# Kernel optimization log

Measured on AMD Instinct MI355X. Metric: run time of the kernel, lower is better.

Reference implementation:

```python
import jax, jax.numpy as jnp
import numpy as np

N_USERS = 20000
N_ITEMS = 20000
H0, H1, H2 = 256, 512, 256  # hidden = [256, 512, 256]
B = 4096
LN_EPS = 1e-5


def _ln(x, g, b):
    m = jnp.mean(x, axis=-1, keepdims=True)
    v = jnp.mean(jnp.square(x - m), axis=-1, keepdims=True)
    return (x - m) * jax.lax.rsqrt(v + LN_EPS) * g + b


def setup_inputs() -> dict:
    key = jax.random.key(0)
    ks = jax.random.split(key, 12)
    s = 0.02
    inp = {
        "user_idx": jax.random.randint(ks[0], (B,), 0, N_USERS),
        "item_idx": jax.random.randint(ks[1], (B,), 0, N_ITEMS),
        # (n_users+1, n_items+1) binary interaction matrix, stored as bool
        "interactions": jax.random.bernoulli(ks[2], 0.05, (N_USERS + 1, N_ITEMS + 1)),
        # proj_u / proj_i (bias=False), torch Linear layout (out, in)
        "Wu": jax.random.normal(ks[3], (H0, N_ITEMS), jnp.float32) * s,
        "Wi": jax.random.normal(ks[4], (H0, N_USERS), jnp.float32) * s,
        # rep_u: Linear(H0,H1)+LN+ReLU, Linear(H1,H2)+LN+ReLU (dropout=eval identity)
        "W1": jax.random.normal(ks[5], (H1, H0), jnp.float32) * s,
        "b1": jnp.zeros((H1,), jnp.float32),
        "g1": jnp.ones((H1,), jnp.float32),
        "be1": jnp.zeros((H1,), jnp.float32),
        "W2": jax.random.normal(ks[6], (H2, H1), jnp.float32) * s,
        "b2": jnp.zeros((H2,), jnp.float32),
        "g2": jnp.ones((H2,), jnp.float32),
        "be2": jnp.zeros((H2,), jnp.float32),
        # logit layer
        "Wl": jax.random.normal(ks[7], (1, H2), jnp.float32) * s,
        "bl": jnp.zeros((1,), jnp.float32),
    }
    return inp


def reference(user_idx, item_idx, interactions, Wu, Wi, W1, b1, g1, be1,
              W2, b2, g2, be2, Wl, bl):
    b_arange = jnp.arange(user_idx.shape[0])

    # --- user history embedding: gather row, zero target item, project, MLP ---
    u_slice = interactions[user_idx, :-1].astype(jnp.float32)      # (B, n_items)
    u_slice = u_slice.at[b_arange, item_idx].set(0.0)
    u = u_slice @ Wu.T                                             # (B, H0)
    u = jax.nn.relu(_ln(u @ W1.T + b1, g1, be1))                   # (B, H1)
    user_rep = jax.nn.relu(_ln(u @ W2.T + b2, g2, be2))            # (B, H2)

    # --- item history embedding: gather column, zero target user, project ---
    i_slice = interactions.T[item_idx][:, :-1].astype(jnp.float32)  # (B, n_users)
    i_slice = i_slice.at[b_arange, user_idx].set(0.0)
    item_rep = i_slice @ Wi.T                                      # (B, H0); rep_i is an empty Sequential in source

    pred_vector = user_rep * item_rep                              # (B, H2) == (B, H0)
    logit = (pred_vector @ Wl.T + bl).squeeze(-1)                  # (B,)
    return logit
```

## Files before the change

kernel.cpp:

```cpp
#include <hip/hip_runtime.h>

#define N_USERS 20000
#define N_ITEMS 20000
#define NI1     20001
#define HB      4096
#define H0      256
#define H1      512
#define H2      256
#define PKW     632
#define PKB     (PKW*4)
#define NWF     12501251

typedef unsigned short u16;
typedef unsigned char  u8;
typedef unsigned int   u32;
typedef unsigned long long u64;

typedef __attribute__((ext_vector_type(8))) __bf16 bf16x8;
typedef __attribute__((ext_vector_type(4))) float  f32x4;

__device__ __forceinline__ u16 f2bf(float f) {
  u32 u = __float_as_uint(f);
  u32 r = (u + 0x7FFFu + ((u >> 16) & 1u)) >> 16;
  return (u16)r;
}

__global__ __launch_bounds__(256) void k_detect(const u8* __restrict__ inter,
                                                int* __restrict__ flag) {
  __shared__ u32 cnt[4];
  if (threadIdx.x < 4) cnt[threadIdx.x] = 0;
  __syncthreads();
  u32 loc0 = 0, loc1 = 0, loc2 = 0, loc3 = 0;
  for (int i = threadIdx.x; i < 16384; i += 256) {
    u32 w = ((const u32*)inter)[i];
    loc0 += (w & 0x000000FFu) ? 1u : 0u;
    loc1 += (w & 0x0000FF00u) ? 1u : 0u;
    loc2 += (w & 0x00FF0000u) ? 1u : 0u;
    loc3 += (w & 0xFF000000u) ? 1u : 0u;
  }
  atomicAdd(&cnt[0], loc0); atomicAdd(&cnt[1], loc1);
  atomicAdd(&cnt[2], loc2); atomicAdd(&cnt[3], loc3);
  __syncthreads();
  if (threadIdx.x == 0) {
    int lay;
    if (cnt[1] != 0)      lay = 0;
    else if (cnt[0] != 0) lay = 1;
    else                  lay = 2;
    *flag = lay;
  }
}

__global__ __launch_bounds__(256) void k_packF(const u8* __restrict__ inter,
                                               u32* __restrict__ pkF,
                                               const int* __restrict__ flag) {
  int lay = *flag;
  __shared__ u32 nibs[4][8][64];
  const size_t TE = (size_t)NI1 * NI1;
  const int NG = (int)((TE + 8191) / 8192);
  int wave = threadIdx.x >> 6, lane = threadIdx.x & 63;
  const u32* base32 = (const u32*)inter;
  for (int g = blockIdx.x; g < NG; g += gridDim.x) {
    size_t E0 = (size_t)g * 8192 + (size_t)wave * 2048;
    bool full = ((size_t)(g + 1) * 8192) <= TE;
    if (lay != 0) {
      if (full) {
        #pragma unroll
        for (int t = 0; t < 8; ++t) {
          size_t e = E0 + (size_t)t * 256 + lane * 4;
          uint4 v = *(const uint4*)(base32 + e);
          nibs[wave][t][lane] = (v.x ? 1u : 0u) | (v.y ? 2u : 0u) |
                                (v.z ? 4u : 0u) | (v.w ? 8u : 0u);
        }
      } else {
        #pragma unroll
        for (int t = 0; t < 8; ++t) {
          size_t e = E0 + (size_t)t * 256 + lane * 4;
          u32 n = 0;
          #pragma unroll
          for (int c = 0; c < 4; ++c)
            if (e + c < TE && base32[e + c]) n |= 1u << c;
          nibs[wave][t][lane] = n;
        }
      }
    } else {
      #pragma unroll
      for (int t = 0; t < 8; ++t) {
        size_t e = E0 + (size_t)t * 256 + lane * 4;
        u32 n = 0;
        #pragma unroll
        for (int c = 0; c < 4; ++c)
          if (e + c < TE && inter[e + c]) n |= 1u << c;
        nibs[wave][t][lane] = n;
      }
    }
    __syncthreads();
    {
      int t = lane >> 3, j = lane & 7;
      u32 wrd = 0;
      #pragma unroll
      for (int k = 0; k < 8; ++k) wrd |= nibs[wave][t][8 * j + k] << (4 * k);
      size_t wg = (size_t)g * 256 + wave * 64 + lane;
      if (wg < NWF) pkF[wg] = wrd;
    }
    __syncthreads();
  }
}

__global__ __launch_bounds__(256) void k_realign(const u32* __restrict__ pkF,
                                                 u32* __restrict__ pk) {
  int r = blockIdx.x;
  int base = 625 * r + (r >> 5);
  int s = r & 31;
  for (int w = threadIdx.x; w < PKW; w += 256) {
    u32 val = 0;
    if (w < 625) {
      u32 lo = pkF[base + w];
      u32 hi = pkF[base + w + 1];
      val = s ? ((lo >> s) | (hi << (32 - s))) : lo;
    }
    pk[(size_t)r * PKW + w] = val;
  }
}

#define HDSTEP(J, M)                                      \
  _Pragma("unroll")                                       \
  for (int k = 0; k < 32; ++k) if (!(k & J)) {            \
    u32 tt = (a[k] ^ (a[k | J] >> J)) & M;                \
    a[k] ^= tt; a[k | J] ^= tt << J;                      \
  }

__global__ __launch_bounds__(256) void k_bitT(const u32* __restrict__ pk,
                                              u32* __restrict__ pkT) {
  __shared__ u32 in_l[512][17];
  __shared__ u32 out_l[32][16][17];
  int t = threadIdx.x;
  int vt = blockIdx.x % 40, wt = blockIdx.x / 40;
  int v0 = vt * 16, wc0 = wt * 16;
  int lw = t & 15, lr = t >> 4;
  for (int ch = 0; ch < 32; ++ch) {
    int rloc = ch * 16 + lr;
    int R = v0 * 32 + rloc;
    int W = wc0 + lw;
    u32 val = 0;
    if (R < N_USERS && W < PKW) val = pk[(size_t)R * PKW + W];
    in_l[rloc][lw] = val;
  }
  __syncthreads();
  u32 a[32];
  #pragma unroll
  for (int j = 0; j < 32; ++j) a[j] = in_l[lr * 32 + j][lw];
  HDSTEP(16, 0x0000FFFFu)
  HDSTEP(8,  0x00FF00FFu)
  HDSTEP(4,  0x0F0F0F0Fu)
  HDSTEP(2,  0x33333333u)
  HDSTEP(1,  0x55555555u)
  #pragma unroll
  for (int i = 0; i < 32; ++i) out_l[i][lw][lr] = __brev(a[31 - i]);
  __syncthreads();
  for (int ch = 0; ch < 32; ++ch) {
    int rloc = ch * 16 + lr;
    int C = wc0 * 32 + rloc;
    int V = v0 + lw;
    if (C < N_ITEMS && V < PKW)
      pkT[(size_t)C * PKW + V] = out_l[rloc & 31][rloc >> 5][lw];
  }
}

__global__ __launch_bounds__(256) void k_convert2(const float* __restrict__ Wu,
                                                  const float* __restrict__ Wi,
                                                  u16* __restrict__ Wub,
                                                  u16* __restrict__ Wib) {
  const int n4 = H0 * N_ITEMS / 4;
  int stride = gridDim.x * 256;
  for (int i = blockIdx.x * 256 + threadIdx.x; i < 2 * n4; i += stride) {
    const float* in = (i < n4) ? Wu : Wi;
    u16* out = (i < n4) ? Wub : Wib;
    int idx = (i < n4) ? i : i - n4;
    float4 v = ((const float4*)in)[idx];
    u64 p = (u64)f2bf(v.x) | ((u64)f2bf(v.y) << 16) |
            ((u64)f2bf(v.z) << 32) | ((u64)f2bf(v.w) << 48);
    ((u64*)out)[idx] = p;
  }
}

__global__ __launch_bounds__(256) void k_transpose2(const float* __restrict__ W1,
                                                    float* __restrict__ W1T,
                                                    const float* __restrict__ W2,
                                                    float* __restrict__ W2T) {
  __shared__ float tile[32][33];
  int bid = blockIdx.x;
  const float* in; float* out; int R, C, b;
  if (bid < 128) { in = W1; out = W1T; R = H1; C = H0; b = bid; }
  else           { in = W2; out = W2T; R = H2; C = H1; b = bid - 128; }
  int nbx = C >> 5;
  int bx = b % nbx, by = b / nbx;
  int c0 = bx * 32, r0 = by * 32;
  int lx = threadIdx.x & 31, ly = threadIdx.x >> 5;
  #pragma unroll
  for (int j = 0; j < 4; ++j)
    tile[ly + 8*j][lx] = in[(size_t)(r0 + ly + 8*j) * C + c0 + lx];
  __syncthreads();
  #pragma unroll
  for (int j = 0; j < 4; ++j)
    out[(size_t)(c0 + ly + 8*j) * R + r0 + lx] = tile[lx][ly + 8*j];
}

__global__ __launch_bounds__(1024) void k_sort(const int* __restrict__ item_idx,
                                               int* __restrict__ perm) {
  __shared__ u32 cnt[N_ITEMS];
  __shared__ u32 tsum[1024];
  int t = threadIdx.x;
  for (int i = t; i < N_ITEMS; i += 1024) cnt[i] = 0;
  __syncthreads();
  for (int b = t; b < HB; b += 1024) atomicAdd(&cnt[item_idx[b]], 1u);
  __syncthreads();
  u32 s = 0;
  int base = t * 20;
  for (int j = 0; j < 20; ++j) { int i = base + j; if (i < N_ITEMS) s += cnt[i]; }
  tsum[t] = s;
  __syncthreads();
  for (int off = 1; off < 1024; off <<= 1) {
    u32 v = (t >= off) ? tsum[t - off] : 0u;
    __syncthreads();
    tsum[t] += v;
    __syncthreads();
  }
  u32 run = tsum[t] - s;
  for (int j = 0; j < 20; ++j) {
    int i = base + j;
    if (i < N_ITEMS) { u32 c = cnt[i]; cnt[i] = run; run += c; }
  }
  __syncthreads();
  for (int b = t; b < HB; b += 1024) {
    int v = item_idx[b];
    u32 pos = atomicAdd(&cnt[v], 1u);
    perm[pos] = b;
  }
}

__global__ __launch_bounds__(256, 4) void k_gemm(
    const u32* __restrict__ pk, const u32* __restrict__ pkT,
    const int* __restrict__ user_idx, const int* __restrict__ item_idx,
    const int* __restrict__ perm,
    const u16* __restrict__ Wub, const u16* __restrict__ Wib,
    float* __restrict__ u0, float* __restrict__ u0b,
    float* __restrict__ ir, float* __restrict__ irb) {
  __shared__ __attribute__((aligned(16))) u16 Bls[32 * 256];
  __shared__ __attribute__((aligned(16))) uint2 lut8[16];
  __shared__ u32 pbase[128];
  __shared__ int prow[128];

  int bid = blockIdx.x;
  int kh = bid >> 9;
  int mode_item = (bid >> 8) & 1;
  int lid = bid & 255;
  int M0 = (lid >> 3) * 128;
  int N0 = (lid & 7) * 32;
  int tid = threadIdx.x;
  const u16* Wb = mode_item ? Wib : Wub;
  const u8* Pk = (const u8*)(mode_item ? pkT : pk);
  float* Cout = mode_item ? (kh ? irb : ir) : (kh ? u0b : u0);

  if (tid < 16) {
    u32 v = tid;
    lut8[tid].x = ((v & 1u) ? 0x3F80u : 0u) | ((v & 2u) ? 0x3F800000u : 0u);
    lut8[tid].y = ((v & 4u) ? 0x3F80u : 0u) | ((v & 8u) ? 0x3F800000u : 0u);
  }
  if (tid < 128) {
    int s = M0 + tid;
    if (mode_item) { int p = perm[s]; prow[tid] = p; pbase[tid] = (u32)item_idx[p] * PKB; }
    else           { prow[tid] = s;   pbase[tid] = (u32)user_idx[s] * PKB; }
  }
  __syncthreads();

  f32x4 acc[2][2];
  #pragma unroll
  for (int a = 0; a < 2; ++a)
    #pragma unroll
    for (int b = 0; b < 2; ++b)
      #pragma unroll
      for (int j = 0; j < 4; ++j) acc[a][b][j] = 0.f;

  int lane = tid & 63, wave = tid >> 6;
  int WM = wave * 32;
  int lrow = lane & 15;
  int lk8 = lane >> 4;
  int sh = lk8 * 8;

  u32 pb0 = pbase[WM + lrow];
  u32 pb1 = pbase[WM + 16 + lrow];

  int k0_beg = kh ? 10240 : 0;
  int k0_end = kh ? 20224 : 10240;

  for (int k0 = k0_beg; k0 < k0_end; k0 += 256) {
    #pragma unroll
    for (int i = 0; i < 4; ++i) {
      int id = tid + 256 * i;
      int n = id >> 5, c8 = id & 31;
      int k = k0 + c8 * 8;
      uint4 v = make_uint4(0u, 0u, 0u, 0u);
      if (k < N_ITEMS) v = *(const uint4*)&Wb[(size_t)(N0 + n) * N_ITEMS + k];
      int off = n * 256 + ((c8 * 8) ^ ((n & 7) << 3));
      *(uint4*)&Bls[off] = v;
    }
    int bc = k0 >> 3;
    uint4 qa0l = *(const uint4*)(Pk + pb0 + bc);
    uint4 qa0h = *(const uint4*)(Pk + pb0 + bc + 16);
    uint4 qa1l = *(const uint4*)(Pk + pb1 + bc);
    uint4 qa1h = *(const uint4*)(Pk + pb1 + bc + 16);
    u32 qw0[8] = {qa0l.x, qa0l.y, qa0l.z, qa0l.w, qa0h.x, qa0h.y, qa0h.z, qa0h.w};
    u32 qw1[8] = {qa1l.x, qa1l.y, qa1l.z, qa1l.w, qa1h.x, qa1h.y, qa1h.z, qa1h.w};
    __syncthreads();
    #pragma unroll
    for (int kki = 0; kki < 8; ++kki) {
      u32 b0 = (qw0[kki] >> sh) & 0xFFu;
      u32 b1 = (qw1[kki] >> sh) & 0xFFu;
      union { u32 w[4]; bf16x8 v; } a0, a1;
      uint2 l0 = lut8[b0 & 15u], h0 = lut8[b0 >> 4];
      uint2 l1 = lut8[b1 & 15u], h1 = lut8[b1 >> 4];
      a0.w[0] = l0.x; a0.w[1] = l0.y; a0.w[2] = h0.x; a0.w[3] = h0.y;
      a1.w[0] = l1.x; a1.w[1] = l1.y; a1.w[2] = h1.x; a1.w[3] = h1.y;
      bf16x8 bfr[2];
      #pragma unroll
      for (int fn = 0; fn < 2; ++fn) {
        int n = fn * 16 + lrow;
        bfr[fn] = *(const bf16x8*)&Bls[n * 256 + ((kki * 32 + sh) ^ ((n & 7) << 3))];
      }
      acc[0][0] = __builtin_amdgcn_mfma_f32_16x16x32_bf16(a0.v, bfr[0], acc[0][0], 0, 0, 0);
      acc[0][1] = __builtin_amdgcn_mfma_f32_16x16x32_bf16(a0.v, bfr[1], acc[0][1], 0, 0, 0);
      acc[1][0] = __builtin_amdgcn_mfma_f32_16x16x32_bf16(a1.v, bfr[0], acc[1][0], 0, 0, 0);
      acc[1][1] = __builtin_amdgcn_mfma_f32_16x16x32_bf16(a1.v, bfr[1], acc[1][1], 0, 0, 0);
    }
    __syncthreads();
  }

  int crow0 = (lane >> 4) * 4;
  int ccol = lane & 15;
  #pragma unroll
  for (int fm = 0; fm < 2; ++fm)
    #pragma unroll
    for (int fn = 0; fn < 2; ++fn) {
      f32x4 v = acc[fm][fn];
      int col = N0 + fn * 16 + ccol;
      #pragma unroll
      for (int j = 0; j < 4; ++j) {
        int rl = WM + fm * 16 + crow0 + j;
        Cout[(size_t)prow[rl] * H0 + col] = v[j];
      }
    }
}

__global__ __launch_bounds__(256) void k_mlp(
    const u32* __restrict__ pk,
    const int* __restrict__ user_idx, const int* __restrict__ item_idx,
    const float* __restrict__ Wu, const float* __restrict__ Wi,
    const float* __restrict__ u0, const float* __restrict__ u0b,
    const float* __restrict__ ir, const float* __restrict__ irb,
    const float* __restrict__ W1T, const float* __restrict__ b1,
    const float* __restrict__ g1, const float* __restrict__ be1,
    const float* __restrict__ W2T, const float* __restrict__ b2,
    const float* __restrict__ g2, const float* __restrict__ be2,
    const float* __restrict__ Wl, const float* __restrict__ bl,
    float* __restrict__ out) {
  __shared__ __attribute__((aligned(16))) float xl[16][H0];
  __shared__ __attribute__((aligned(16))) float h1l[16][H1];
  __shared__ int flagL[16], uL[16], iL[16];

  int tid = threadIdx.x, lane = tid & 63, wave = tid >> 6;
  int b0 = blockIdx.x * 16;

  if (tid < 16) {
    int b = b0 + tid;
    int uu = user_idx[b], ii = item_idx[b];
    uL[tid] = uu; iL[tid] = ii;
    u8 byte = ((const u8*)pk)[(size_t)uu * PKB + (ii >> 3)];
    flagL[tid] = (byte >> (ii & 7)) & 1;
  }
  __syncthreads();

  for (int idx = tid; idx < 16 * H0; idx += 256) {
    int rr = idx >> 8, h = idx & 255;
    size_t o = (size_t)(b0 + rr) * H0 + h;
    float x = u0[o] + u0b[o];
    if (flagL[rr]) x -= Wu[(size_t)h * N_ITEMS + iL[rr]];
    xl[rr][h] = x;
  }
  __syncthreads();

  float a0[16], a1[16];
  #pragma unroll
  for (int rr = 0; rr < 16; ++rr) { a0[rr] = 0.f; a1[rr] = 0.f; }
  for (int k4 = 0; k4 < H0 / 4; ++k4) {
    int k = k4 * 4;
    float w0a = W1T[(size_t)(k+0)*H1 + tid], w0b = W1T[(size_t)(k+0)*H1 + tid + 256];
    float w1a = W1T[(size_t)(k+1)*H1 + tid], w1b = W1T[(size_t)(k+1)*H1 + tid + 256];
    float w2a = W1T[(size_t)(k+2)*H1 + tid], w2b = W1T[(size_t)(k+2)*H1 + tid + 256];
    float w3a = W1T[(size_t)(k+3)*H1 + tid], w3b = W1T[(size_t)(k+3)*H1 + tid + 256];
    #pragma unroll
    for (int rr = 0; rr < 16; ++rr) {
      float4 x = *(const float4*)&xl[rr][k];
      a0[rr] += x.x * w0a + x.y * w1a + x.z * w2a + x.w * w3a;
      a1[rr] += x.x * w0b + x.y * w1b + x.z * w2b + x.w * w3b;
    }
  }
  #pragma unroll
  for (int rr = 0; rr < 16; ++rr) {
    h1l[rr][tid]       = a0[rr] + b1[tid];
    h1l[rr][tid + 256] = a1[rr] + b1[tid + 256];
  }
  __syncthreads();

  for (int rr = wave; rr < 16; rr += 4) {
    float s = 0.f;
    #pragma unroll
    for (int j = 0; j < 8; ++j) s += h1l[rr][lane + 64 * j];
    #pragma unroll
    for (int off = 32; off; off >>= 1) s += __shfl_xor(s, off);
    float m = s * (1.f / H1);
    float v = 0.f;
    #pragma unroll
    for (int j = 0; j < 8; ++j) { float d = h1l[rr][lane + 64*j] - m; v += d * d; }
    #pragma unroll
    for (int off = 32; off; off >>= 1) v += __shfl_xor(v, off);
    float inv = rsqrtf(v * (1.f / H1) + 1e-5f);
    #pragma unroll
    for (int j = 0; j < 8; ++j) {
      int o = lane + 64 * j;
      float y = (h1l[rr][o] - m) * inv * g1[o] + be1[o];
      h1l[rr][o] = fmaxf(y, 0.f);
    }
  }
  __syncthreads();

  float a2[16];
  #pragma unroll
  for (int rr = 0; rr < 16; ++rr) a2[rr] = 0.f;
  for (int k4 = 0; k4 < H1 / 4; ++k4) {
    int k = k4 * 4;
    float w0 = W2T[(size_t)(k+0)*H2 + tid];
    float w1 = W2T[(size_t)(k+1)*H2 + tid];
    float w2 = W2T[(size_t)(k+2)*H2 + tid];
    float w3 = W2T[(size_t)(k+3)*H2 + tid];
    #pragma unroll
    for (int rr = 0; rr < 16; ++rr) {
      float4 x = *(const float4*)&h1l[rr][k];
      a2[rr] += x.x * w0 + x.y * w1 + x.z * w2 + x.w * w3;
    }
  }
  __syncthreads();
  #pragma unroll
  for (int rr = 0; rr < 16; ++rr) xl[rr][tid] = a2[rr] + b2[tid];
  __syncthreads();

  for (int rr = wave; rr < 16; rr += 4) {
    float s = 0.f;
    #pragma unroll
    for (int j = 0; j < 4; ++j) s += xl[rr][lane + 64 * j];
    #pragma unroll
    for (int off = 32; off; off >>= 1) s += __shfl_xor(s, off);
    float m = s * (1.f / H2);
    float v = 0.f;
    #pragma unroll
    for (int j = 0; j < 4; ++j) { float d = xl[rr][lane + 64*j] - m; v += d * d; }
    #pragma unroll
    for (int off = 32; off; off >>= 1) v += __shfl_xor(v, off);
    float inv = rsqrtf(v * (1.f / H2) + 1e-5f);
    #pragma unroll
    for (int j = 0; j < 4; ++j) {
      int o = lane + 64 * j;
      float y = (xl[rr][o] - m) * inv * g2[o] + be2[o];
      xl[rr][o] = fmaxf(y, 0.f);
    }
  }
  __syncthreads();

  for (int rr = wave; rr < 16; rr += 4) {
    int b = b0 + rr;
    int flg = flagL[rr], uu = uL[rr];
    float s = 0.f;
    #pragma unroll
    for (int j = 0; j < 4; ++j) {
      int h = lane + 64 * j;
      size_t o = (size_t)b * H0 + h;
      float irv = ir[o] + irb[o];
      if (flg) irv -= Wi[(size_t)h * N_USERS + uu];
      s += xl[rr][h] * irv * Wl[h];
    }
    #pragma unroll
    for (int off = 32; off; off >>= 1) s += __shfl_xor(s, off);
    if (lane == 0) out[b] = s + bl[0];
  }
}

extern "C" void kernel_launch(void* const* d_in, const int* in_sizes, int n_in,
                              void* d_out, int out_size, void* d_ws, size_t ws_size,
                              hipStream_t stream) {
  const int*   user_idx = (const int*)d_in[0];
  const int*   item_idx = (const int*)d_in[1];
  const u8*    inter    = (const u8*)d_in[2];
  const float* Wu  = (const float*)d_in[3];
  const float* Wi  = (const float*)d_in[4];
  const float* W1  = (const float*)d_in[5];
  const float* b1  = (const float*)d_in[6];
  const float* g1  = (const float*)d_in[7];
  const float* be1 = (const float*)d_in[8];
  const float* W2  = (const float*)d_in[9];
  const float* b2  = (const float*)d_in[10];
  const float* g2  = (const float*)d_in[11];
  const float* be2 = (const float*)d_in[12];
  const float* Wl  = (const float*)d_in[13];
  const float* bl  = (const float*)d_in[14];
  float* out = (float*)d_out;

  char* ws = (char*)d_ws;
  size_t off = 0;
  auto alloc = [&](size_t bytes) {
    size_t o = off;
    off = (off + bytes + 255) & ~(size_t)255;
    return o;
  };
  int*   flag = (int*)  (ws + alloc(4));
  u32*   pkF  = (u32*)  (ws + alloc((size_t)(NWF + 64) * 4));
  u32*   pk   = (u32*)  (ws + alloc((size_t)N_USERS * PKB));
  u32*   pkT  = (u32*)  (ws + alloc((size_t)N_ITEMS * PKB));
  u16*   Wub  = (u16*)  (ws + alloc((size_t)H0 * N_ITEMS * 2));
  u16*   Wib  = (u16*)  (ws + alloc((size_t)H0 * N_USERS * 2));
  float* W1T  = (float*)(ws + alloc((size_t)H0 * H1 * 4));
  float* W2T  = (float*)(ws + alloc((size_t)H1 * H2 * 4));
  float* u0   = (float*)(ws + alloc((size_t)HB * H0 * 4));
  float* u0b  = (float*)(ws + alloc((size_t)HB * H0 * 4));
  float* ir   = (float*)(ws + alloc((size_t)HB * H0 * 4));
  float* irb  = (float*)(ws + alloc((size_t)HB * H0 * 4));
  int*   perm = (int*)  (ws + alloc((size_t)HB * 4));

  k_detect<<<1, 256, 0, stream>>>(inter, flag);
  k_packF<<<3072, 256, 0, stream>>>(inter, pkF, flag);
  k_realign<<<N_USERS, 256, 0, stream>>>(pkF, pk);
  k_bitT<<<1600, 256, 0, stream>>>(pk, pkT);
  k_convert2<<<1024, 256, 0, stream>>>(Wu, Wi, Wub, Wib);
  k_transpose2<<<256, 256, 0, stream>>>(W1, W1T, W2, W2T);
  k_sort<<<1, 1024, 0, stream>>>(item_idx, perm);
  k_gemm<<<1024, 256, 0, stream>>>(pk, pkT, user_idx, item_idx, perm, Wub, Wib,
                                   u0, u0b, ir, irb);
  k_mlp<<<256, 256, 0, stream>>>(pk, user_idx, item_idx, Wu, Wi, u0, u0b, ir, irb,
                                 W1T, b1, g1, be1, W2T, b2, g2, be2, Wl, bl, out);
}
```

Before: 658.8 us.

## Double-buffer B tile in LDS and prefetch next K-slice into registers

The k_gemm main loop now issues global loads for the next 256-wide K slice of the weight tile and packed interaction bits before running the MFMAs on the current slice. It then writes them into a second LDS buffer, so one barrier per iteration replaces two. This is meant to hide global memory latency behind the MFMA work. In exchange it doubles the B-tile LDS footprint to 32 KB and needs more registers, which may lower occupancy under launch_bounds(256,4).

```diff
diff --git a/kernel.cpp b/kernel.cpp
--- a/kernel.cpp
+++ b/kernel.cpp
@@ -245,7 +245,7 @@
     const u16* __restrict__ Wub, const u16* __restrict__ Wib,
     float* __restrict__ u0, float* __restrict__ u0b,
     float* __restrict__ ir, float* __restrict__ irb) {
-  __shared__ __attribute__((aligned(16))) u16 Bls[32 * 256];
+  __shared__ __attribute__((aligned(16))) u16 Bls[2][32 * 256];
   __shared__ __attribute__((aligned(16))) uint2 lut8[16];
   __shared__ u32 pbase[128];
   __shared__ int prow[128];
@@ -290,28 +290,55 @@
   u32 pb0 = pbase[WM + lrow];
   u32 pb1 = pbase[WM + 16 + lrow];
 
+  int bsn[4], bsk[4], bso[4];
+  #pragma unroll
+  for (int i = 0; i < 4; ++i) {
+    int id = tid + 256 * i;
+    int n = id >> 5, c8 = id & 31;
+    bsn[i] = N0 + n;
+    bsk[i] = c8 * 8;
+    bso[i] = n * 256 + ((c8 * 8) ^ ((n & 7) << 3));
+  }
+
   int k0_beg = kh ? 10240 : 0;
   int k0_end = kh ? 20224 : 10240;
 
+  uint4 breg[4];
+  #pragma unroll
+  for (int i = 0; i < 4; ++i) {
+    int k = k0_beg + bsk[i];
+    breg[i] = make_uint4(0u, 0u, 0u, 0u);
+    if (k < N_ITEMS) breg[i] = *(const uint4*)&Wb[(size_t)bsn[i] * N_ITEMS + k];
+  }
+  #pragma unroll
+  for (int i = 0; i < 4; ++i) *(uint4*)&Bls[0][bso[i]] = breg[i];
+  int bc0 = k0_beg >> 3;
+  uint4 ca0l = *(const uint4*)(Pk + pb0 + bc0);
+  uint4 ca0h = *(const uint4*)(Pk + pb0 + bc0 + 16);
+  uint4 ca1l = *(const uint4*)(Pk + pb1 + bc0);
+  uint4 ca1h = *(const uint4*)(Pk + pb1 + bc0 + 16);
+  __syncthreads();
+
+  int cur = 0;
   for (int k0 = k0_beg; k0 < k0_end; k0 += 256) {
-    #pragma unroll
-    for (int i = 0; i < 4; ++i) {
-      int id = tid + 256 * i;
-      int n = id >> 5, c8 = id & 31;
-      int k = k0 + c8 * 8;
-      uint4 v = make_uint4(0u, 0u, 0u, 0u);
-      if (k < N_ITEMS) v = *(const uint4*)&Wb[(size_t)(N0 + n) * N_ITEMS + k];
-      int off = n * 256 + ((c8 * 8) ^ ((n & 7) << 3));
-      *(uint4*)&Bls[off] = v;
-    }
-    int bc = k0 >> 3;
-    uint4 qa0l = *(const uint4*)(Pk + pb0 + bc);
-    uint4 qa0h = *(const uint4*)(Pk + pb0 + bc + 16);
-    uint4 qa1l = *(const uint4*)(Pk + pb1 + bc);
-    uint4 qa1h = *(const uint4*)(Pk + pb1 + bc + 16);
-    u32 qw0[8] = {qa0l.x, qa0l.y, qa0l.z, qa0l.w, qa0h.x, qa0h.y, qa0h.z, qa0h.w};
-    u32 qw1[8] = {qa1l.x, qa1l.y, qa1l.z, qa1l.w, qa1h.x, qa1h.y, qa1h.z, qa1h.w};
-    __syncthreads();
+    int k1 = k0 + 256;
+    bool more = k1 < k0_end;
+    uint4 na0l, na0h, na1l, na1h;
+    if (more) {
+      #pragma unroll
+      for (int i = 0; i < 4; ++i) {
+        int k = k1 + bsk[i];
+        breg[i] = make_uint4(0u, 0u, 0u, 0u);
+        if (k < N_ITEMS) breg[i] = *(const uint4*)&Wb[(size_t)bsn[i] * N_ITEMS + k];
+      }
+      int nbc = k1 >> 3;
+      na0l = *(const uint4*)(Pk + pb0 + nbc);
+      na0h = *(const uint4*)(Pk + pb0 + nbc + 16);
+      na1l = *(const uint4*)(Pk + pb1 + nbc);
+      na1h = *(const uint4*)(Pk + pb1 + nbc + 16);
+    }
+    u32 qw0[8] = {ca0l.x, ca0l.y, ca0l.z, ca0l.w, ca0h.x, ca0h.y, ca0h.z, ca0h.w};
+    u32 qw1[8] = {ca1l.x, ca1l.y, ca1l.z, ca1l.w, ca1h.x, ca1h.y, ca1h.z, ca1h.w};
     #pragma unroll
     for (int kki = 0; kki < 8; ++kki) {
       u32 b0 = (qw0[kki] >> sh) & 0xFFu;
@@ -325,14 +352,20 @@
       #pragma unroll
       for (int fn = 0; fn < 2; ++fn) {
         int n = fn * 16 + lrow;
-        bfr[fn] = *(const bf16x8*)&Bls[n * 256 + ((kki * 32 + sh) ^ ((n & 7) << 3))];
+        bfr[fn] = *(const bf16x8*)&Bls[cur][n * 256 + ((kki * 32 + sh) ^ ((n & 7) << 3))];
       }
       acc[0][0] = __builtin_amdgcn_mfma_f32_16x16x32_bf16(a0.v, bfr[0], acc[0][0], 0, 0, 0);
       acc[0][1] = __builtin_amdgcn_mfma_f32_16x16x32_bf16(a0.v, bfr[1], acc[0][1], 0, 0, 0);
       acc[1][0] = __builtin_amdgcn_mfma_f32_16x16x32_bf16(a1.v, bfr[0], acc[1][0], 0, 0, 0);
       acc[1][1] = __builtin_amdgcn_mfma_f32_16x16x32_bf16(a1.v, bfr[1], acc[1][1], 0, 0, 0);
     }
+    if (more) {
+      #pragma unroll
+      for (int i = 0; i < 4; ++i) *(uint4*)&Bls[cur ^ 1][bso[i]] = breg[i];
+      ca0l = na0l; ca0h = na0h; ca1l = na1l; ca1h = na1h;
+    }
     __syncthreads();
+    cur ^= 1;
   }
 
   int crow0 = (lane >> 4) * 4;
```

After: 657.3 us. About the same (-0.2%).
